# Kernel tuning notes

Measured on AMD Instinct MI355X. Metric: run time of the kernel, lower is better.

Reference implementation:

```python
import jax, jax.numpy as jnp
import numpy as np

EMBED_DIM = 64
D_STATE = 16
D_CONV = 4
EXPAND = 2
DT_RANK = 8
D_INNER = EXPAND * EMBED_DIM  # 128
B_, T_, H_, W_ = 4, 16, 16, 16


def _causal_dwconv(x, w, b):
    # x: (B, D, L), w: (D, 1, K) depthwise causal conv (left pad K-1), matches
    # torch conv1d(padding=K-1)[..., :L]
    K = w.shape[-1]
    y = jax.lax.conv_general_dilated(
        x, w, window_strides=(1,), padding=[(K - 1, 0)],
        feature_group_count=x.shape[1], dimension_numbers=('NCH', 'OIH', 'NCH'))
    return y + b[None, :, None]


def _selective_scan(u, delta, A, Bm, Cm, D):
    # u, delta: (B, d, L); A: (d, n); Bm, Cm: (B, n, L); D: (d,)
    dA = jnp.exp(jnp.einsum('bdl,dn->lbdn', delta, A))      # (L,B,d,n)
    dBu = jnp.einsum('bdl,bnl,bdl->lbdn', delta, Bm, u)     # (L,B,d,n)
    h0 = jnp.zeros(dA.shape[1:], dA.dtype)

    def step(h, xs):
        dA_t, dBu_t = xs
        h = dA_t * h + dBu_t
        return h, h

    _, hs = jax.lax.scan(step, h0, (dA, dBu))               # (L,B,d,n)
    y = jnp.einsum('lbdn,bnl->bdl', hs, Cm)
    return y + u * D[None, :, None]


def _mamba_branch(x, z, conv_w, conv_b, xproj_w, dtproj_w, dtproj_b, A_log, D):
    # x, z: (B, d_inner, L)
    x = jax.nn.silu(_causal_dwconv(x, conv_w, conv_b))
    x_dbl = jnp.einsum('bdl,ed->bel', x, xproj_w)           # e = dt_rank + 2*n
    dt = x_dbl[:, :DT_RANK]
    Bm = x_dbl[:, DT_RANK:DT_RANK + D_STATE]
    Cm = x_dbl[:, DT_RANK + D_STATE:]
    delta = jax.nn.softplus(jnp.einsum('brl,dr->bdl', dt, dtproj_w) + dtproj_b[None, :, None])
    A = -jnp.exp(A_log)
    y = _selective_scan(x, delta, A, Bm, Cm, D)
    return y * jax.nn.silu(z)


def _conv3d(x, w, b, pad):
    y = jax.lax.conv_general_dilated(
        x, w, window_strides=(1, 1, 1), padding=[(pad, pad)] * 3,
        dimension_numbers=('NCDHW', 'OIDHW', 'NCDHW'))
    return y + b[None, :, None, None, None]


def setup_inputs() -> dict:
    key = jax.random.key(0)
    ks = jax.random.split(key, 24)
    s = 0.02
    d, n, r, K, C = D_INNER, D_STATE, DT_RANK, D_CONV, EMBED_DIM
    inp = {
        'x': jax.random.normal(ks[0], (B_, C, T_, H_, W_), jnp.float32),
        'in_proj_w': jax.random.normal(ks[1], (2 * d, C), jnp.float32) * s,
        'conv_w': jax.random.normal(ks[2], (d, 1, K), jnp.float32) * s,
        'conv_b': jnp.zeros((d,), jnp.float32),
        'xproj_w': jax.random.normal(ks[3], (r + 2 * n, d), jnp.float32) * s,
        'dtproj_w': jax.random.normal(ks[4], (d, r), jnp.float32) * s,
        'dtproj_b': jax.random.normal(ks[5], (d,), jnp.float32) * s,
        'A_log': jnp.tile(jnp.log(jnp.arange(1, n + 1, dtype=jnp.float32))[None, :], (d, 1)),
        'D': jnp.ones((d,), jnp.float32),
        'conv_w_b': jax.random.normal(ks[6], (d, 1, K), jnp.float32) * s,
        'conv_b_b': jnp.zeros((d,), jnp.float32),
        'xproj_w_b': jax.random.normal(ks[7], (r + 2 * n, d), jnp.float32) * s,
        'dtproj_w_b': jax.random.normal(ks[8], (d, r), jnp.float32) * s,
        'dtproj_b_b': jax.random.normal(ks[9], (d,), jnp.float32) * s,
        'A_b_log': jnp.tile(jnp.log(jnp.arange(1, n + 1, dtype=jnp.float32))[None, :], (d, 1)),
        'D_b': jnp.ones((d,), jnp.float32),
        'out_proj_w': jax.random.normal(ks[10], (C, d), jnp.float32) * s,
        'proj_w': jax.random.normal(ks[11], (C, C, 3, 3, 3), jnp.float32) * s,
        'proj_b': jnp.zeros((C,), jnp.float32),
        'norm_w': jax.random.normal(ks[12], (C, C, 1, 1, 1), jnp.float32) * s,
        'norm_b': jnp.zeros((C,), jnp.float32),
    }
    return inp


def reference(x, in_proj_w, conv_w, conv_b, xproj_w, dtproj_w, dtproj_b, A_log, D,
              conv_w_b, conv_b_b, xproj_w_b, dtproj_w_b, dtproj_b_b, A_b_log, D_b,
              out_proj_w, proj_w, proj_b, norm_w, norm_b):
    residual = x
    B, C, T, H, W = x.shape
    # SpectralPriority scan: b c t h w -> b c (h w t)
    seq = x.transpose(0, 1, 3, 4, 2).reshape(B, C, H * W * T)
    # bimamba v2
    xz = jnp.einsum('bcl,ec->bel', seq, in_proj_w)          # (B, 2*d_inner, L)
    x_f, z_f = xz[:, :D_INNER], xz[:, D_INNER:]
    y_f = _mamba_branch(x_f, z_f, conv_w, conv_b, xproj_w, dtproj_w, dtproj_b, A_log, D)
    xz_r = jnp.flip(xz, -1)
    x_b, z_b = xz_r[:, :D_INNER], xz_r[:, D_INNER:]
    y_b = _mamba_branch(x_b, z_b, conv_w_b, conv_b_b, xproj_w_b, dtproj_w_b, dtproj_b_b, A_b_log, D_b)
    out = y_f + jnp.flip(y_b, -1)                           # (B, d_inner, L)
    out = jnp.einsum('bdl,cd->blc', out, out_proj_w)        # (B, L, C)
    x_recon = out.reshape(B, C, T, H, W)
    x3 = _conv3d(x_recon, proj_w, proj_b, pad=1)
    return _conv3d(x3 + residual, norm_w, norm_b, pad=0)
```

## Files before the change

### kernel.cpp

```cpp
#include <hip/hip_runtime.h>


#define NL 4096

typedef unsigned short u16;
typedef unsigned int u32;
typedef __attribute__((ext_vector_type(8))) short bf16x8;
typedef __attribute__((ext_vector_type(4))) float f32x4;

__device__ __forceinline__ float siluf_(float x) {
  return x * __builtin_amdgcn_rcpf(1.f + __expf(-x));
}
__device__ __forceinline__ float softplusf_(float x) {
  return (x > 20.f) ? x : __logf(1.f + __expf(x));
}
__device__ __forceinline__ u16 f2bf(float f) {
  u32 u = __float_as_uint(f);
  u += 0x7fffu + ((u >> 16) & 1u);
  return (u16)(u >> 16);
}
__device__ __forceinline__ float bflo(u32 v) { return __uint_as_float(v << 16); }
__device__ __forceinline__ float bfhi(u32 v) { return __uint_as_float(v & 0xFFFF0000u); }

__device__ __forceinline__ float rowsum16_(float p) {
  int q;
  q = __builtin_amdgcn_mov_dpp(__float_as_int(p), 0x121, 0xf, 0xf, false);
  p += __int_as_float(q);
  q = __builtin_amdgcn_mov_dpp(__float_as_int(p), 0x122, 0xf, 0xf, false);
  p += __int_as_float(q);
  q = __builtin_amdgcn_mov_dpp(__float_as_int(p), 0x124, 0xf, 0xf, false);
  p += __int_as_float(q);
  q = __builtin_amdgcn_mov_dpp(__float_as_int(p), 0x128, 0xf, 0xf, false);
  p += __int_as_float(q);
  return p;
}

#define OXZ  0u
#define OUCF 1048576u
#define OUCB 1572864u
#define ODLF 2424832u
#define ODLB 2949120u
#define OYF  3473408u
#define OYB  3997696u
#define OO   4521984u
#define OO2  5046272u
#define PER_B 5570560u

#define NCH 64
#define CL  64

__global__ __launch_bounds__(256) void kxz(
    const float* __restrict__ x, const float* __restrict__ wip,
    float* __restrict__ ws, int b0) {
  int bi = blockIdx.y, gb = b0 + bi;
  float* s = ws + (size_t)bi * PER_B;
  int bid = blockIdx.x;
  int h = bid >> 4, w = bid & 15;
  int tid = threadIdx.x;
  __shared__ float xs[64][16];
  for (int i = tid; i < 1024; i += 256) {
    int c = i >> 4, t = i & 15;
    xs[c][t] = x[(size_t)(gb * 64 + c) * NL + t * 256 + h * 16 + w];
  }
  __syncthreads();
  int e = tid;
  float acc[16];
#pragma unroll
  for (int t = 0; t < 16; ++t) acc[t] = 0.f;
  for (int c = 0; c < 64; ++c) {
    float wv = wip[e * 64 + c];
#pragma unroll
    for (int t = 0; t < 16; ++t) acc[t] = fmaf(wv, xs[c][t], acc[t]);
  }
  float4* dst = (float4*)(s + OXZ + (size_t)e * NL + h * 256 + w * 16);
#pragma unroll
  for (int q = 0; q < 4; ++q)
    dst[q] = make_float4(acc[q * 4], acc[q * 4 + 1], acc[q * 4 + 2], acc[q * 4 + 3]);
}

__global__ __launch_bounds__(256) void k2prep(
    const float* __restrict__ cwf, const float* __restrict__ cbf,
    const float* __restrict__ xpf, const float* __restrict__ dtwf,
    const float* __restrict__ dtbf,
    const float* __restrict__ cwb, const float* __restrict__ cbb,
    const float* __restrict__ xpb, const float* __restrict__ dtwb,
    const float* __restrict__ dtbb,
    float* __restrict__ ws) {
  int bi = blockIdx.y;
  float* s = ws + (size_t)bi * PER_B;
  int bx = blockIdx.x;
  int lt = bx >> 1, dir = bx & 1;
  int l0 = lt * 32;
  int lout0 = dir ? (127 - lt) * 32 : l0;
  int tid = threadIdx.x;

  __shared__ float pool[128 * 40];
  __shared__ u16 uct[32][136];
  float (*X)[40] = (float(*)[40])pool;

  for (int i = tid; i < 128 * 38; i += 256) {
    int d = i / 38, j = i - d * 38;
    int l = l0 - 3 + j;
    X[d][j] = (l >= 0 && l < NL) ? s[OXZ + (size_t)d * NL + l] : 0.f;
  }
  __syncthreads();

  const float* cw = dir ? cwb : cwf;
  const float* cb = dir ? cbb : cbf;
  u16* ucg = (u16*)(s + (dir ? OUCB : OUCF));
  for (int i = tid; i < 128 * 32; i += 256) {
    int d = i >> 5, li = i & 31;
    float a = cb[d];
    if (dir == 0) {
#pragma unroll
      for (int k = 0; k < 4; ++k) a = fmaf(cw[d * 4 + k], X[d][li + k], a);
    } else {
#pragma unroll
      for (int k = 0; k < 4; ++k) a = fmaf(cw[d * 4 + k], X[d][37 - li - k], a);
    }
    a = siluf_(a);
    u16 ab = f2bf(a);
    uct[li][d] = ab;
    ucg[(size_t)d * NL + lout0 + li] = ab;
  }
  __syncthreads();

  float* xds = pool;
  {
    int wid = tid >> 6, lane = tid & 63;
    int n16 = lane & 15, kg = lane >> 4;
    const float* xp = dir ? xpb : xpf;
#pragma unroll
    for (int rep = 0; rep < 2; ++rep) {
      int id = wid + rep * 4;
      if (id < 6) {
        int et = id >> 1, lt2 = id & 1;
        f32x4 acc = {};
#pragma unroll
        for (int ks = 0; ks < 4; ++ks) {
          bf16x8 bfrag = *(const bf16x8*)&uct[lt2 * 16 + n16][ks * 32 + kg * 8];
          int e = et * 16 + n16;
          int ec = (e < 40) ? e : 39;
          const float* pa = xp + ec * 128 + ks * 32 + kg * 8;
          float4 a0 = *(const float4*)pa;
          float4 a1 = *(const float4*)(pa + 4);
          bf16x8 af;
          af[0] = (short)f2bf(a0.x); af[1] = (short)f2bf(a0.y);
          af[2] = (short)f2bf(a0.z); af[3] = (short)f2bf(a0.w);
          af[4] = (short)f2bf(a1.x); af[5] = (short)f2bf(a1.y);
          af[6] = (short)f2bf(a1.z); af[7] = (short)f2bf(a1.w);
          acc = __builtin_amdgcn_mfma_f32_16x16x32_bf16(af, bfrag, acc, 0, 0, 0);
        }
#pragma unroll
        for (int rg = 0; rg < 4; ++rg) {
          int e = et * 16 + kg * 4 + rg;
          if (e < 40) xds[e * 33 + lt2 * 16 + n16] = acc[rg];
        }
      }
    }
  }
  __syncthreads();

  const float* dtw = dir ? dtwb : dtwf;
  const float* dtb = dir ? dtbb : dtbf;
  u16* dlg = (u16*)(s + (dir ? ODLB : ODLF));
  for (int i = tid; i < 128 * 32; i += 256) {
    int d = i >> 5, li = i & 31;
    float pre = dtb[d];
#pragma unroll
    for (int r = 0; r < 8; ++r)
      pre = fmaf(dtw[d * 8 + r], xds[r * 33 + li], pre);
    dlg[(size_t)d * NL + lout0 + li] = f2bf(softplusf_(pre));
  }
  u16* bctp = (u16*)(s + OO2);
  for (int i = tid; i < 32 * 32; i += 256) {
    int li = i >> 5, k = i & 31;
    bctp[((size_t)dir * 4096 + lout0 + li) * 32 + k] = f2bf(xds[(8 + k) * 33 + li]);
  }
}

__global__ __launch_bounds__(256) void kscanA(
    const float* __restrict__ Alf, const float* __restrict__ Alb,
    float* __restrict__ ws) {
  int bi = blockIdx.y;
  float* s = ws + (size_t)bi * PER_B;
  int xid = blockIdx.x;
  int chunk = xid >> 4, dir = (xid >> 3) & 1, d8 = xid & 7;
  int tid = threadIdx.x;
  int wv = tid >> 6, lane = tid & 63;
  int n = lane & 15, g = lane >> 4;
  int d = d8 * 16 + wv * 4 + g;
  int l0 = chunk * CL;
  __shared__ float bl[CL * 32];
  {
    const u16* bctp = (const u16*)(s + OO2) + ((size_t)dir * 4096 + l0) * 32;
    for (int i = tid; i < CL * 32; i += 256)
      bl[i] = __uint_as_float(((u32)bctp[i]) << 16);
  }
  __syncthreads();
  const u16* ucp = (const u16*)(s + (dir ? OUCB : OUCF)) + (size_t)d * NL + l0;
  const u16* dlp = (const u16*)(s + (dir ? ODLB : ODLF)) + (size_t)d * NL + l0;
  float A = -__expf((dir ? Alb : Alf)[d * 16 + n]);
  float P = 1.f, S = 0.f;
  for (int i0 = 0; i0 < CL; i0 += 8) {
    uint4 dq = *(const uint4*)(dlp + i0);
    uint4 uq = *(const uint4*)(ucp + i0);
    float dv[8] = {bflo(dq.x), bfhi(dq.x), bflo(dq.y), bfhi(dq.y),
                   bflo(dq.z), bfhi(dq.z), bflo(dq.w), bfhi(dq.w)};
    float uv[8] = {bflo(uq.x), bfhi(uq.x), bflo(uq.y), bfhi(uq.y),
                   bflo(uq.z), bfhi(uq.z), bflo(uq.w), bfhi(uq.w)};
#pragma unroll
    for (int j = 0; j < 8; ++j) {
      float dA = __expf(dv[j] * A);
      S = fmaf(dA, S, dv[j] * bl[(i0 + j) * 32 + n] * uv[j]);
      P *= dA;
    }
  }
  size_t cidx = ((size_t)(chunk * 2 + dir) * 128 + d) * 16 + n;
  s[OO + cidx] = P;
  s[OO + 262144u + cidx] = S;
}

__global__ __launch_bounds__(64) void kscanB(float* __restrict__ ws) {
  int bi = blockIdx.y;
  float* s = ws + (size_t)bi * PER_B;
  int dir = blockIdx.x >> 5, dblk = blockIdx.x & 31;
  int tid = threadIdx.x;
  size_t base = (size_t)dir * 2048 + dblk * 64 + tid;
  float carry = 0.f;
#pragma unroll 4
  for (int c = 0; c < NCH; ++c) {
    size_t idx = (size_t)c * 4096 + base;
    float pv = s[OO + idx], sv = s[OO + 262144u + idx];
    s[OO + 262144u + idx] = carry;
    carry = fmaf(pv, carry, sv);
  }
}

__global__ __launch_bounds__(256) void kscanC(
    const float* __restrict__ Alf, const float* __restrict__ Df,
    const float* __restrict__ Alb, const float* __restrict__ Db,
    float* __restrict__ ws) {
  int bi = blockIdx.y;
  float* s = ws + (size_t)bi * PER_B;
  int xid = blockIdx.x;
  int chunk = xid >> 4, dir = (xid >> 3) & 1, d8 = xid & 7;
  int tid = threadIdx.x;
  int wv = tid >> 6, lane = tid & 63;
  int n = lane & 15, g = lane >> 4;
  int d = d8 * 16 + wv * 4 + g;
  int l0 = chunk * CL;
  __shared__ float bl[CL * 32];
  __shared__ float ps[16][65];
  {
    const u16* bctp = (const u16*)(s + OO2) + ((size_t)dir * 4096 + l0) * 32;
    for (int i = tid; i < CL * 32; i += 256)
      bl[i] = __uint_as_float(((u32)bctp[i]) << 16);
  }
  __syncthreads();
  const u16* ucp = (const u16*)(s + (dir ? OUCB : OUCF)) + (size_t)d * NL + l0;
  const u16* dlp = (const u16*)(s + (dir ? ODLB : ODLF)) + (size_t)d * NL + l0;
  float* ybase = s + (dir ? OYB : OYF);
  float A = -__expf((dir ? Alb : Alf)[d * 16 + n]);
  float Dv = (dir ? Db : Df)[d];
  size_t cidx = ((size_t)(chunk * 2 + dir) * 128 + d) * 16 + n;
  float h = s[OO + 262144u + cidx];
  int prow = wv * 4 + g;
  for (int i0 = 0; i0 < CL; i0 += 8) {
    uint4 dq = *(const uint4*)(dlp + i0);
    uint4 uq = *(const uint4*)(ucp + i0);
    float dv[8] = {bflo(dq.x), bfhi(dq.x), bflo(dq.y), bfhi(dq.y),
                   bflo(dq.z), bfhi(dq.z), bflo(dq.w), bfhi(dq.w)};
    float uv[8] = {bflo(uq.x), bfhi(uq.x), bflo(uq.y), bfhi(uq.y),
                   bflo(uq.z), bfhi(uq.z), bflo(uq.w), bfhi(uq.w)};
#pragma unroll
    for (int j = 0; j < 8; ++j) {
      int i = i0 + j;
      float dA = __expf(dv[j] * A);
      h = fmaf(dA, h, dv[j] * bl[i * 32 + n] * uv[j]);
      float p = rowsum16_(h * bl[i * 32 + 16 + n]);
      if (n == 0) ps[prow][i] = fmaf(uv[j], Dv, p);
    }
  }
  __syncthreads();
  for (int i = tid; i < 16 * CL; i += 256) {
    int row = i >> 6, col = i & 63;
    ybase[(size_t)(d8 * 16 + row) * NL + l0 + col] = ps[row][col];
  }
}

__global__ __launch_bounds__(256) void koutg(
    const float* __restrict__ wout, float* __restrict__ ws) {
  int bi = blockIdx.y;
  float* s = ws + (size_t)bi * PER_B;
  int lt = blockIdx.x;
  int l0 = lt * 32;
  int tid = threadIdx.x;
  __shared__ u16 otb[32][136];
  for (int i = tid; i < 128 * 32; i += 256) {
    int d = i >> 5, li = i & 31;
    int l = l0 + li;
    float z = s[OXZ + (size_t)(128 + d) * NL + l];
    float v = s[OYF + (size_t)d * NL + l] + s[OYB + (size_t)d * NL + (NL - 1 - l)];
    otb[li][d] = f2bf(v * siluf_(z));
  }
  __syncthreads();
  int wid = tid >> 6, lane = tid & 63;
  int n16 = lane & 15, kg = lane >> 4;
  f32x4 acc[2] = {};
  const float* wr = wout + (size_t)(wid * 16 + n16) * 128 + kg * 8;
#pragma unroll
  for (int ks = 0; ks < 4; ++ks) {
    const float* pa = wr + ks * 32;
    float4 a0 = *(const float4*)pa;
    float4 a1 = *(const float4*)(pa + 4);
    bf16x8 af;
    af[0] = (short)f2bf(a0.x); af[1] = (short)f2bf(a0.y);
    af[2] = (short)f2bf(a0.z); af[3] = (short)f2bf(a0.w);
    af[4] = (short)f2bf(a1.x); af[5] = (short)f2bf(a1.y);
    af[6] = (short)f2bf(a1.z); af[7] = (short)f2bf(a1.w);
    bf16x8 b0 = *(const bf16x8*)&otb[n16][ks * 32 + kg * 8];
    bf16x8 b1 = *(const bf16x8*)&otb[16 + n16][ks * 32 + kg * 8];
    acc[0] = __builtin_amdgcn_mfma_f32_16x16x32_bf16(af, b0, acc[0], 0, 0, 0);
    acc[1] = __builtin_amdgcn_mfma_f32_16x16x32_bf16(af, b1, acc[1], 0, 0, 0);
  }
#pragma unroll
  for (int l2 = 0; l2 < 2; ++l2) {
    float4 st = make_float4(acc[l2][0], acc[l2][1], acc[l2][2], acc[l2][3]);
    *(float4*)&s[OO2 + (size_t)(l0 + l2 * 16 + n16) * 64 + wid * 16 + kg * 4] = st;
  }
}

__global__ __launch_bounds__(256) void kprepw(
    const float* __restrict__ pw, float* __restrict__ wdst) {
  int off = blockIdx.x;
  u16* wb = (u16*)wdst;
  int tid = threadIdx.x;
  for (int i = tid; i < 4096; i += 256) {
    int co = i >> 6, ci = i & 63;
    wb[off * 4096 + i] = f2bf(pw[(size_t)(co * 64 + ci) * 27 + off]);
  }
}

__global__ __launch_bounds__(256) void kconv3(
    const float* __restrict__ pb, const float* __restrict__ nw,
    const float* __restrict__ nb, const float* __restrict__ xin,
    float* __restrict__ out, const u16* __restrict__ wb,
    float* __restrict__ ws, int b0) {
  int bi = blockIdx.y, gb = b0 + bi;
  float* s = ws + (size_t)bi * PER_B;
  int t = blockIdx.x >> 2, hq = blockIdx.x & 3;
  int h0 = hq * 4;
  int tid = threadIdx.x;
  const float* xr = s + OO2;

  __shared__ u16 Xs[3 * 6 * 18 * 72];
  float* cx = (float*)Xs;
  {
    u32* xz32 = (u32*)Xs;
    for (int i = tid; i < 3 * 6 * 18 * 72 / 2; i += 256) xz32[i] = 0u;
  }
  __syncthreads();
  {
    int ci = tid >> 2, wq = tid & 3;
    for (int row = 0; row < 18; ++row) {
      int tt = row / 6, hh = row - tt * 6;
      int ts = t + tt - 1, hs = h0 + hh - 1;
      if (ts < 0 || ts > 15 || hs < 0 || hs > 15) continue;
      float4 v = *(const float4*)(xr + (size_t)ci * NL + ts * 256 + hs * 16 + wq * 4);
      int rb = (tt * 6 + hh) * 18 + 1 + wq * 4;
      Xs[(rb + 0) * 72 + ci] = f2bf(v.x);
      Xs[(rb + 1) * 72 + ci] = f2bf(v.y);
      Xs[(rb + 2) * 72 + ci] = f2bf(v.z);
      Xs[(rb + 3) * 72 + ci] = f2bf(v.w);
    }
  }
  __syncthreads();

  int wid = tid >> 6, lane = tid & 63;
  int cb = wid >> 1, lb = wid & 1;
  int n16 = lane & 15, kg = lane >> 4;
  f32x4 acc[2][2] = {};

  const u16* wbA = wb + (size_t)(cb * 32 + n16) * 64 + kg * 8;
  for (int kt = 0; kt < 3; ++kt)
    for (int kh = 0; kh < 3; ++kh) {
      int rbase = (kt * 6 + lb * 2 + kh) * 18 + n16;
#pragma unroll
      for (int kw = 0; kw < 3; ++kw) {
        int off = (kt * 3 + kh) * 3 + kw;
        int r0 = rbase + kw;
        const u16* pa = wbA + off * 4096;
#pragma unroll
        for (int st = 0; st < 2; ++st) {
          int kb = st * 32;
          bf16x8 a0 = *(const bf16x8*)(pa + kb);
          bf16x8 a1 = *(const bf16x8*)(pa + 16 * 64 + kb);
          bf16x8 b0 = *(const bf16x8*)(&Xs[r0 * 72 + kb + kg * 8]);
          bf16x8 b1 = *(const bf16x8*)(&Xs[(r0 + 18) * 72 + kb + kg * 8]);
          acc[0][0] = __builtin_amdgcn_mfma_f32_16x16x32_bf16(a0, b0, acc[0][0], 0, 0, 0);
          acc[0][1] = __builtin_amdgcn_mfma_f32_16x16x32_bf16(a0, b1, acc[0][1], 0, 0, 0);
          acc[1][0] = __builtin_amdgcn_mfma_f32_16x16x32_bf16(a1, b0, acc[1][0], 0, 0, 0);
          acc[1][1] = __builtin_amdgcn_mfma_f32_16x16x32_bf16(a1, b1, acc[1][1], 0, 0, 0);
        }
      }
    }
  __syncthreads();

#pragma unroll
  for (int c2 = 0; c2 < 2; ++c2) {
#pragma unroll
    for (int l2 = 0; l2 < 2; ++l2) {
      int lp = (lb * 2 + l2) * 16 + n16;
      int lg = t * 256 + h0 * 16 + lp;
#pragma unroll
      for (int rg = 0; rg < 4; ++rg) {
        int co = cb * 32 + c2 * 16 + kg * 4 + rg;
        cx[co * 65 + lp] = acc[c2][l2][rg] + pb[co] +
                           xin[(size_t)(gb * 64 + co) * NL + lg];
      }
    }
  }
  __syncthreads();

  {
    int co2 = tid >> 2, pq = tid & 3;
    float mac[16];
#pragma unroll
    for (int j = 0; j < 16; ++j) mac[j] = 0.f;
    for (int ci = 0; ci < 64; ci += 4) {
      float4 w4 = *(const float4*)&nw[co2 * 64 + ci];
      float wv[4] = {w4.x, w4.y, w4.z, w4.w};
#pragma unroll
      for (int cc = 0; cc < 4; ++cc) {
        const float* row = &cx[(ci + cc) * 65 + pq * 16];
        float4 a = *(const float4*)&row[0];
        float4 b = *(const float4*)&row[4];
        float4 c = *(const float4*)&row[8];
        float4 e = *(const float4*)&row[12];
        mac[0] = fmaf(wv[cc], a.x, mac[0]);   mac[1] = fmaf(wv[cc], a.y, mac[1]);
        mac[2] = fmaf(wv[cc], a.z, mac[2]);   mac[3] = fmaf(wv[cc], a.w, mac[3]);
        mac[4] = fmaf(wv[cc], b.x, mac[4]);   mac[5] = fmaf(wv[cc], b.y, mac[5]);
        mac[6] = fmaf(wv[cc], b.z, mac[6]);   mac[7] = fmaf(wv[cc], b.w, mac[7]);
        mac[8] = fmaf(wv[cc], c.x, mac[8]);   mac[9] = fmaf(wv[cc], c.y, mac[9]);
        mac[10] = fmaf(wv[cc], c.z, mac[10]); mac[11] = fmaf(wv[cc], c.w, mac[11]);
        mac[12] = fmaf(wv[cc], e.x, mac[12]); mac[13] = fmaf(wv[cc], e.y, mac[13]);
        mac[14] = fmaf(wv[cc], e.z, mac[14]); mac[15] = fmaf(wv[cc], e.w, mac[15]);
      }
    }
    float bias = nb[co2];
    float4* dst = (float4*)(out + (size_t)(gb * 64 + co2) * NL +
                            t * 256 + h0 * 16 + pq * 16);
#pragma unroll
    for (int q = 0; q < 4; ++q)
      dst[q] = make_float4(mac[q * 4] + bias, mac[q * 4 + 1] + bias,
                           mac[q * 4 + 2] + bias, mac[q * 4 + 3] + bias);
  }
}

extern "C" void kernel_launch(void* const* d_in, const int* in_sizes, int n_in,
                              void* d_out, int out_size, void* d_ws, size_t ws_size,
                              hipStream_t stream) {
  const float* x    = (const float*)d_in[0];
  const float* wip  = (const float*)d_in[1];
  const float* cwf  = (const float*)d_in[2];
  const float* cbf  = (const float*)d_in[3];
  const float* xpf  = (const float*)d_in[4];
  const float* dtwf = (const float*)d_in[5];
  const float* dtbf = (const float*)d_in[6];
  const float* Alf  = (const float*)d_in[7];
  const float* Df   = (const float*)d_in[8];
  const float* cwb  = (const float*)d_in[9];
  const float* cbb  = (const float*)d_in[10];
  const float* xpb  = (const float*)d_in[11];
  const float* dtwb = (const float*)d_in[12];
  const float* dtbb = (const float*)d_in[13];
  const float* Alb  = (const float*)d_in[14];
  const float* Db   = (const float*)d_in[15];
  const float* wout = (const float*)d_in[16];
  const float* pw   = (const float*)d_in[17];
  const float* pb   = (const float*)d_in[18];
  const float* nw   = (const float*)d_in[19];
  const float* nb   = (const float*)d_in[20];

  const size_t PER_B_BYTES = (size_t)PER_B * 4;
  const size_t WB_BYTES = 27u * 64u * 64u * 2u;
  int bcnt;
  if (ws_size >= 4 * PER_B_BYTES + WB_BYTES) bcnt = 4;
  else if (ws_size >= PER_B_BYTES + WB_BYTES) bcnt = 1;
  else return;
  int passes = 4 / bcnt;

  float* ws = (float*)d_ws;
  float* wsW = ws + (size_t)bcnt * PER_B;
  kprepw<<<dim3(27), 256, 0, stream>>>(pw, wsW);
  for (int p = 0; p < passes; ++p) {
    int b0 = p * bcnt;
    kxz   <<<dim3(256, bcnt), 256, 0, stream>>>(x, wip, ws, b0);
    k2prep<<<dim3(256, bcnt), 256, 0, stream>>>(cwf, cbf, xpf, dtwf, dtbf,
                                                cwb, cbb, xpb, dtwb, dtbb, ws);
    kscanA<<<dim3(1024, bcnt), 256, 0, stream>>>(Alf, Alb, ws);
    kscanB<<<dim3(64, bcnt), 64, 0, stream>>>(ws);
    kscanC<<<dim3(1024, bcnt), 256, 0, stream>>>(Alf, Df, Alb, Db, ws);
    koutg <<<dim3(128, bcnt), 256, 0, stream>>>(wout, ws);
    kconv3<<<dim3(64, bcnt), 256, 0, stream>>>(pb, nw, nb, x, (float*)d_out,
                                               (const u16*)wsW, ws, b0);
  }
}
```

Baseline: 265.0 us.

## Replicate conv3d bf16 weights per XCD and retile waves over output channels

The weight prep kernel now writes eight copies of the bf16 3D-conv weights, and each conv3 block reads the copy chosen by blockIdx mod 8. The apparent intent is to keep the weights local to each XCD's L2 and avoid cross-die traffic. Each wave now owns 16 output channels across all 4 spatial rows, with one A fragment feeding 4 MFMAs instead of a 2x2 channel-by-row tile. The loops are fully unrolled and launch bounds set to one block per SM, which raises register use and may limit occupancy. Workspace for weights grows eightfold.

```diff
diff --git a/kernel.cpp b/kernel.cpp
--- a/kernel.cpp
+++ b/kernel.cpp
@@ -48,6 +48,7 @@
 
 #define NCH 64
 #define CL  64
+#define WB1 110592u
 
 __global__ __launch_bounds__(256) void kxz(
     const float* __restrict__ x, const float* __restrict__ wip,
@@ -338,18 +339,22 @@
   int tid = threadIdx.x;
   for (int i = tid; i < 4096; i += 256) {
     int co = i >> 6, ci = i & 63;
-    wb[off * 4096 + i] = f2bf(pw[(size_t)(co * 64 + ci) * 27 + off]);
-  }
-}
-
-__global__ __launch_bounds__(256) void kconv3(
+    u16 v = f2bf(pw[(size_t)(co * 64 + ci) * 27 + off]);
+#pragma unroll
+    for (int xc = 0; xc < 8; ++xc)
+      wb[(size_t)xc * WB1 + off * 4096 + i] = v;
+  }
+}
+
+__global__ __launch_bounds__(256, 1) void kconv3(
     const float* __restrict__ pb, const float* __restrict__ nw,
     const float* __restrict__ nb, const float* __restrict__ xin,
     float* __restrict__ out, const u16* __restrict__ wb,
     float* __restrict__ ws, int b0) {
   int bi = blockIdx.y, gb = b0 + bi;
   float* s = ws + (size_t)bi * PER_B;
-  int t = blockIdx.x >> 2, hq = blockIdx.x & 3;
+  int bx = blockIdx.x;
+  int t = bx >> 2, hq = bx & 3;
   int h0 = hq * 4;
   int tid = threadIdx.x;
   const float* xr = s + OO2;
@@ -378,47 +383,44 @@
   __syncthreads();
 
   int wid = tid >> 6, lane = tid & 63;
-  int cb = wid >> 1, lb = wid & 1;
+  int cq = wid;
   int n16 = lane & 15, kg = lane >> 4;
-  f32x4 acc[2][2] = {};
-
-  const u16* wbA = wb + (size_t)(cb * 32 + n16) * 64 + kg * 8;
+  f32x4 acc[4] = {};
+
+  const u16* wbA = wb + (size_t)(bx & 7) * WB1 +
+                   (size_t)(cq * 16 + n16) * 64 + kg * 8;
+#pragma unroll
   for (int kt = 0; kt < 3; ++kt)
+#pragma unroll
     for (int kh = 0; kh < 3; ++kh) {
-      int rbase = (kt * 6 + lb * 2 + kh) * 18 + n16;
 #pragma unroll
       for (int kw = 0; kw < 3; ++kw) {
         int off = (kt * 3 + kh) * 3 + kw;
-        int r0 = rbase + kw;
         const u16* pa = wbA + off * 4096;
 #pragma unroll
         for (int st = 0; st < 2; ++st) {
           int kb = st * 32;
           bf16x8 a0 = *(const bf16x8*)(pa + kb);
-          bf16x8 a1 = *(const bf16x8*)(pa + 16 * 64 + kb);
-          bf16x8 b0 = *(const bf16x8*)(&Xs[r0 * 72 + kb + kg * 8]);
-          bf16x8 b1 = *(const bf16x8*)(&Xs[(r0 + 18) * 72 + kb + kg * 8]);
-          acc[0][0] = __builtin_amdgcn_mfma_f32_16x16x32_bf16(a0, b0, acc[0][0], 0, 0, 0);
-          acc[0][1] = __builtin_amdgcn_mfma_f32_16x16x32_bf16(a0, b1, acc[0][1], 0, 0, 0);
-          acc[1][0] = __builtin_amdgcn_mfma_f32_16x16x32_bf16(a1, b0, acc[1][0], 0, 0, 0);
-          acc[1][1] = __builtin_amdgcn_mfma_f32_16x16x32_bf16(a1, b1, acc[1][1], 0, 0, 0);
+#pragma unroll
+          for (int l2 = 0; l2 < 4; ++l2) {
+            int r = (kt * 6 + l2 + kh) * 18 + n16 + kw;
+            bf16x8 b0 = *(const bf16x8*)(&Xs[r * 72 + kb + kg * 8]);
+            acc[l2] = __builtin_amdgcn_mfma_f32_16x16x32_bf16(a0, b0, acc[l2], 0, 0, 0);
+          }
         }
       }
     }
   __syncthreads();
 
 #pragma unroll
-  for (int c2 = 0; c2 < 2; ++c2) {
-#pragma unroll
-    for (int l2 = 0; l2 < 2; ++l2) {
-      int lp = (lb * 2 + l2) * 16 + n16;
-      int lg = t * 256 + h0 * 16 + lp;
-#pragma unroll
-      for (int rg = 0; rg < 4; ++rg) {
-        int co = cb * 32 + c2 * 16 + kg * 4 + rg;
-        cx[co * 65 + lp] = acc[c2][l2][rg] + pb[co] +
-                           xin[(size_t)(gb * 64 + co) * NL + lg];
-      }
+  for (int l2 = 0; l2 < 4; ++l2) {
+    int lp = l2 * 16 + n16;
+    int lg = t * 256 + (h0 + l2) * 16 + n16;
+#pragma unroll
+    for (int rg = 0; rg < 4; ++rg) {
+      int co = cq * 16 + kg * 4 + rg;
+      cx[co * 65 + lp] = acc[l2][rg] + pb[co] +
+                         xin[(size_t)(gb * 64 + co) * NL + lg];
     }
   }
   __syncthreads();
@@ -484,7 +486,7 @@
   const float* nb   = (const float*)d_in[20];
 
   const size_t PER_B_BYTES = (size_t)PER_B * 4;
-  const size_t WB_BYTES = 27u * 64u * 64u * 2u;
+  const size_t WB_BYTES = 8u * WB1 * 2u;
   int bcnt;
   if (ws_size >= 4 * PER_B_BYTES + WB_BYTES) bcnt = 4;
   else if (ws_size >= PER_B_BYTES + WB_BYTES) bcnt = 1;
```

Measured after the change: 260.6 us. Within noise of the previous version (-1.6%).
